# Optimization experiments

Hardware: AMD Instinct MI355X
Metric: run time of the kernel (lower is better)

## Reference

```python
import jax, jax.numpy as jnp
import numpy as np

E = 400000          # num edges
N_ATOMS = 16000     # num atoms
N_GRAPHS = 256      # num crystals in batch
D_EDGE = 128        # emb_size_edge (== emb_size)
D_RBF = 16          # emb_size_rbf
SILU_SCALE = 1.0 / 0.6  # gemnet ScaledSiLU


def setup_inputs() -> dict:
    key = jax.random.key(0)
    ks = jax.random.split(key, 10)
    edge_emb = jax.random.normal(ks[0], (E, D_EDGE), dtype=jnp.float32)
    distance_vec = jax.random.normal(ks[1], (E, 3), dtype=jnp.float32)
    lattice = jax.random.normal(ks[2], (N_GRAPHS, 3, 3), dtype=jnp.float32)
    rbf = jax.random.uniform(ks[3], (E, D_RBF), dtype=jnp.float32)
    edge_index = jax.random.randint(ks[4], (2, E), 0, N_ATOMS, dtype=jnp.int64)
    batch = jnp.sort(jax.random.randint(ks[5], (N_ATOMS,), 0, N_GRAPHS, dtype=jnp.int64))
    # learned params (gemnet Dense: bias=False)
    def w(k, fan_in, fan_out):
        return jax.random.normal(k, (fan_in, fan_out), dtype=jnp.float32) / np.sqrt(fan_in)
    W1 = w(ks[6], D_EDGE, D_EDGE)       # mlp dense 1 (ScaledSiLU)
    W2 = w(ks[7], D_EDGE, D_EDGE)       # mlp dense 2 (linear)
    W_rbf = w(ks[8], D_RBF, D_EDGE)     # dense_rbf_F
    W_out = w(ks[9], D_EDGE, 1)         # out_forces (num_heads=1)
    return {"edge_emb": edge_emb, "distance_vec": distance_vec, "lattice": lattice,
            "rbf": rbf, "W1": W1, "W2": W2, "W_rbf": W_rbf, "W_out": W_out,
            "edge_index": edge_index, "batch": batch}


def reference(edge_emb, distance_vec, lattice, rbf, W1, W2, W_rbf, W_out, edge_index, batch):
    num_graphs = lattice.shape[0]
    # compute_score_per_edge: MLP(edge_emb) gated by RBF embedding
    x_F = (jax.nn.silu(edge_emb @ W1) * SILU_SCALE) @ W2      # [E, D_EDGE]
    rbf_emb_F = rbf @ W_rbf                                    # [E, D_EDGE]
    edge_scores = (x_F * rbf_emb_F) @ W_out                    # [E, 1]
    # normalize_score=True: divide by number of edges in each graph
    batch_edge = batch[edge_index[0]]                          # [E] graph id per edge
    num_edges = jax.ops.segment_sum(jnp.ones((edge_scores.shape[0],), edge_scores.dtype),
                                    batch_edge, num_segments=num_graphs)
    edge_scores = edge_scores / num_edges[batch_edge][:, None]
    # edge_score_to_lattice_score_frac_symmetric (single head)
    s = edge_scores[:, 0]                                      # [E]
    unit = distance_vec / jnp.linalg.norm(distance_vec, axis=-1, keepdims=True)
    per_edge = jnp.einsum("e,ei,ej->eij", s, unit, distance_vec)  # [E,3,3]
    L = jax.ops.segment_sum(per_edge, batch_edge, num_segments=num_graphs)  # [B,3,3]
    L = 0.5 * (L + jnp.swapaxes(L, -1, -2))                    # symmetrize
    return L
```

## Files before the change

### kernel.cpp

```cpp
#include <hip/hip_runtime.h>
#include <hip/hip_bf16.h>

#define E_EDGES 400000
#define DE      128
#define DRBF    16
#define NG      256
#define TE      64
#define NTILES  (E_EDGES / TE)
#define SILU_SC (1.0f / 0.6f)
#define GRID_MAIN 1568

static_assert(E_EDGES % TE == 0, "tile divisibility");

typedef short bf16x8 __attribute__((ext_vector_type(8)));
typedef float f32x4  __attribute__((ext_vector_type(4)));

__device__ __forceinline__ unsigned int f2bf(float x) {
    union { float f; unsigned int u; } v; v.f = x;
    return (v.u + 0x7FFFu + ((v.u >> 16) & 1u)) >> 16;
}
__device__ __forceinline__ float silu_s(float h) {
    return h / (1.0f + __expf(-h)) * SILU_SC;
}


__global__ __launch_bounds__(256) void gn_prep(
    const float* __restrict__ W1, const float* __restrict__ W2,
    const float* __restrict__ Wr, const float* __restrict__ Wo,
    unsigned char* __restrict__ fragW1, unsigned char* __restrict__ fragG)
{
    const int tid = threadIdx.x, lane = tid & 63, wid = tid >> 6;
    const int lq = lane >> 4, lr = lane & 15, wcol = wid * 32;
    #pragma unroll
    for (int n = 0; n < 2; ++n) {
        const int col = wcol + n * 16 + lr;
        #pragma unroll
        for (int kt = 0; kt < 4; ++kt) {
            bf16x8 v;
            #pragma unroll
            for (int j = 0; j < 8; ++j)
                v[j] = (short)f2bf(W1[(kt * 32 + lq * 8 + j) * DE + col]);
            *reinterpret_cast<bf16x8*>(fragW1 + tid * 128 + (n * 4 + kt) * 16) = v;
        }
        bf16x8 vg = {0, 0, 0, 0, 0, 0, 0, 0};
        if (lq < 2) {
            #pragma unroll
            for (int jj = 0; jj < 8; ++jj) {
                const int j = lq * 8 + jj;
                f32x4 a4 = {0.0f, 0.0f, 0.0f, 0.0f};
                for (int c4 = 0; c4 < 32; ++c4) {
                    const f32x4 w2 = *reinterpret_cast<const f32x4*>(W2 + col * DE + c4 * 4);
                    const f32x4 wr = *reinterpret_cast<const f32x4*>(Wr + j * DE + c4 * 4);
                    const f32x4 wo = *reinterpret_cast<const f32x4*>(Wo + c4 * 4);
                    a4 += w2 * wr * wo;
                }
                vg[jj] = (short)f2bf(a4[0] + a4[1] + a4[2] + a4[3]);
            }
        }
        *reinterpret_cast<bf16x8*>(fragG + tid * 32 + n * 16) = vg;
    }
}

__global__ void gn_count(const int* __restrict__ ei0, const int* __restrict__ batch,
                         int* __restrict__ counts) {
    __shared__ int hist[NG];
    const int tid = threadIdx.x;
    hist[tid] = 0;
    __syncthreads();
    for (int e = blockIdx.x * 256 + tid; e < E_EDGES; e += gridDim.x * 256)
        atomicAdd(&hist[batch[ei0[e]]], 1);
    __syncthreads();
    if (hist[tid]) atomicAdd(&counts[tid], hist[tid]);
}

__global__ __launch_bounds__(256, 3) void gn_main(
    const float* __restrict__ edge_emb, const float* __restrict__ dvec,
    const float* __restrict__ rbf, const int* __restrict__ ei0,
    const int* __restrict__ batch, const int* __restrict__ counts,
    const unsigned char* __restrict__ fragW1, const unsigned char* __restrict__ fragG,
    float* __restrict__ Lws)
{
    __shared__ __align__(16) unsigned char sA[2][TE * DE * 2];
    __shared__ __align__(16) unsigned char sR[2][TE * DRBF * 2];
    __shared__ float sS[2][4][TE];
    __shared__ float sLacc[NG * 9];

    const int tid = threadIdx.x, lane = tid & 63, wid = tid >> 6;
    const int lq = lane >> 4, lr = lane & 15;

    for (int i = tid; i < NG * 9; i += 256) sLacc[i] = 0.0f;

    bf16x8 b1[2][4], bG[2];
    #pragma unroll
    for (int n = 0; n < 2; ++n) {
        #pragma unroll
        for (int kt = 0; kt < 4; ++kt)
            b1[n][kt] = *reinterpret_cast<const bf16x8*>(fragW1 + tid * 128 + (n * 4 + kt) * 16);
        bG[n] = *reinterpret_cast<const bf16x8*>(fragG + tid * 32 + n * 16);
    }

    const f32x4 zero4 = {0.0f, 0.0f, 0.0f, 0.0f};

    {
        const int t0 = blockIdx.x;
        if (t0 < NTILES) {
            const size_t e0 = (size_t)t0 * TE;
            #pragma unroll
            for (int i = 0; i < 8; ++i) {
                const int f4 = i * 256 + tid, row = f4 >> 5, c4 = (f4 & 31) << 2;
                const float4 v = *reinterpret_cast<const float4*>(edge_emb + (e0 + row) * DE + c4);
                uint2 p; p.x = f2bf(v.x) | (f2bf(v.y) << 16); p.y = f2bf(v.z) | (f2bf(v.w) << 16);
                *reinterpret_cast<uint2*>(&sA[0][(row * 256 + c4 * 2) ^ ((row & 7) << 4)]) = p;
            }
            const int row = tid >> 2, ch = tid & 3;
            const float4 v = *reinterpret_cast<const float4*>(rbf + (e0 + row) * DRBF + ch * 4);
            uint2 p; p.x = f2bf(v.x) | (f2bf(v.y) << 16); p.y = f2bf(v.z) | (f2bf(v.w) << 16);
            *reinterpret_cast<uint2*>(&sR[0][row * 32 + ch * 8]) = p;
        }
    }
    __syncthreads();

    int cur = 0;
    for (int t = blockIdx.x; t < NTILES; t += GRID_MAIN) {
        const int tn = t + GRID_MAIN;
        const bool pf = tn < NTILES;

        float4 ve[8], vr;
        if (pf) {
            const size_t e0n = (size_t)tn * TE;
            #pragma unroll
            for (int i = 0; i < 8; ++i) {
                const int f4 = i * 256 + tid, row = f4 >> 5, c4 = (f4 & 31) << 2;
                ve[i] = *reinterpret_cast<const float4*>(edge_emb + (e0n + row) * DE + c4);
            }
            vr = *reinterpret_cast<const float4*>(rbf + (e0n + (tid >> 2)) * DRBF + (tid & 3) * 4);
        }
        int g = 0; float cinv = 0.0f, dx = 0.0f, dy = 0.0f, dz = 0.0f;
        if (tid < TE) {
            const size_t e = (size_t)t * TE + tid;
            g = batch[ei0[e]];
            cinv = 1.0f / (float)counts[g];
            dx = dvec[3 * e]; dy = dvec[3 * e + 1]; dz = dvec[3 * e + 2];
        }

        f32x4 acc[4][2];
        #pragma unroll
        for (int m = 0; m < 4; ++m) { acc[m][0] = zero4; acc[m][1] = zero4; }
        #pragma unroll
        for (int kt = 0; kt < 4; ++kt) {
            bf16x8 a[4];
            #pragma unroll
            for (int m = 0; m < 4; ++m) {
                const int row = m * 16 + lr;
                a[m] = *reinterpret_cast<const bf16x8*>(
                    &sA[cur][(row * 256 + kt * 64 + lq * 16) ^ ((row & 7) << 4)]);
            }
            #pragma unroll
            for (int m = 0; m < 4; ++m) {
                acc[m][0] = __builtin_amdgcn_mfma_f32_16x16x32_bf16(a[m], b1[0][kt], acc[m][0], 0, 0, 0);
                acc[m][1] = __builtin_amdgcn_mfma_f32_16x16x32_bf16(a[m], b1[1][kt], acc[m][1], 0, 0, 0);
            }
        }

        #pragma unroll
        for (int m = 0; m < 4; ++m) {
            bf16x8 aR = {0, 0, 0, 0, 0, 0, 0, 0};
            if (lq < 2)
                aR = *reinterpret_cast<const bf16x8*>(&sR[cur][(m * 16 + lr) * 32 + lq * 16]);
            const f32x4 y0 = __builtin_amdgcn_mfma_f32_16x16x32_bf16(aR, bG[0], zero4, 0, 0, 0);
            const f32x4 y1 = __builtin_amdgcn_mfma_f32_16x16x32_bf16(aR, bG[1], zero4, 0, 0, 0);
            f32x4 p;
            #pragma unroll
            for (int r = 0; r < 4; ++r)
                p[r] = silu_s(acc[m][0][r]) * y0[r] + silu_s(acc[m][1][r]) * y1[r];
            #pragma unroll
            for (int off = 1; off < 16; off <<= 1)
                #pragma unroll
                for (int r = 0; r < 4; ++r)
                    p[r] += __shfl_xor(p[r], off, 64);
            if (lr == 0) {
                #pragma unroll
                for (int r = 0; r < 4; ++r)
                    sS[cur][wid][m * 16 + lq * 4 + r] = p[r];
            }
        }

        if (pf) {
            #pragma unroll
            for (int i = 0; i < 8; ++i) {
                const int f4 = i * 256 + tid, row = f4 >> 5, c4 = (f4 & 31) << 2;
                uint2 p; p.x = f2bf(ve[i].x) | (f2bf(ve[i].y) << 16);
                p.y = f2bf(ve[i].z) | (f2bf(ve[i].w) << 16);
                *reinterpret_cast<uint2*>(&sA[cur ^ 1][(row * 256 + c4 * 2) ^ ((row & 7) << 4)]) = p;
            }
            const int row = tid >> 2, ch = tid & 3;
            uint2 p; p.x = f2bf(vr.x) | (f2bf(vr.y) << 16); p.y = f2bf(vr.z) | (f2bf(vr.w) << 16);
            *reinterpret_cast<uint2*>(&sR[cur ^ 1][row * 32 + ch * 8]) = p;
        }

        __syncthreads();

        if (tid < TE) {
            float s = (sS[cur][0][tid] + sS[cur][1][tid] + sS[cur][2][tid] + sS[cur][3][tid]) * cinv;
            const float rn = 1.0f / sqrtf(dx * dx + dy * dy + dz * dz);
            const float sx = s * dx * rn, sy = s * dy * rn, sz = s * dz * rn;
            float* L = sLacc + g * 9;
            atomicAdd(L + 0, sx * dx); atomicAdd(L + 1, sx * dy); atomicAdd(L + 2, sx * dz);
            atomicAdd(L + 3, sy * dx); atomicAdd(L + 4, sy * dy); atomicAdd(L + 5, sy * dz);
            atomicAdd(L + 6, sz * dx); atomicAdd(L + 7, sz * dy); atomicAdd(L + 8, sz * dz);
        }
        cur ^= 1;
    }

    __syncthreads();
    for (int i = tid; i < NG * 9; i += 256)
        atomicAdd(&Lws[i], sLacc[i]);
}

__global__ void gn_finalize(const float* __restrict__ Lws, float* __restrict__ out) {
    const int i = blockIdx.x * 256 + threadIdx.x;
    if (i < NG * 9) {
        const int g = i / 9, rem = i % 9, r = rem / 3, c = rem % 3;
        out[i] = 0.5f * (Lws[i] + Lws[g * 9 + c * 3 + r]);
    }
}

extern "C" void kernel_launch(void* const* d_in, const int* in_sizes, int n_in,
                              void* d_out, int out_size, void* d_ws, size_t ws_size,
                              hipStream_t stream) {
    const float* edge_emb = (const float*)d_in[0];
    const float* dvec     = (const float*)d_in[1];
    const float* rbf      = (const float*)d_in[3];
    const float* W1       = (const float*)d_in[4];
    const float* W2       = (const float*)d_in[5];
    const float* Wr       = (const float*)d_in[6];
    const float* Wo       = (const float*)d_in[7];
    const int*   ei0      = (const int*)d_in[8];
    const int*   batch    = (const int*)d_in[9];
    float* out = (float*)d_out;

    int*   counts = (int*)d_ws;
    float* Lws    = (float*)((char*)d_ws + 1024);
    unsigned char* fragW1 = (unsigned char*)d_ws + 10240;
    unsigned char* fragG  = (unsigned char*)d_ws + 43008;

    hipMemsetAsync(d_ws, 0, 10240, stream);
    gn_prep<<<1, 256, 0, stream>>>(W1, W2, Wr, Wo, fragW1, fragG);
    gn_count<<<256, 256, 0, stream>>>(ei0, batch, counts);
    gn_main<<<GRID_MAIN, 256, 0, stream>>>(edge_emb, dvec, rbf, ei0, batch, counts,
                                           fragW1, fragG, Lws);
    gn_finalize<<<9, 256, 0, stream>>>(Lws, out);
}
```

Measured before the change: 491.4 us.

## Give each wavefront its own 16-edge tile with full W1 held in registers

The main kernel now assigns each wavefront an independent 16-edge tile and has it hold all of W1's bf16 fragments (8 column blocks by 4 k-steps) in registers. Edge embeddings are loaded from global memory straight into MFMA operand registers, which removes the LDS staging buffers, the double-buffer prefetch and the per-tile block barrier. The prep kernel is spread over 32 small blocks and the fused W2·Wrbf·Wout fragments are now read from global memory on each tile. In exchange, register pressure rises (occupancy hint drops from 3 to 2 blocks), there is no explicit prefetch, and edge rows are read with a less coalesced pattern that relies on the cache.

```diff
diff --git a/kernel.cpp b/kernel.cpp
--- a/kernel.cpp
+++ b/kernel.cpp
@@ -5,12 +5,12 @@
 #define DE      128
 #define DRBF    16
 #define NG      256
-#define TE      64
-#define NTILES  (E_EDGES / TE)
+#define MT      16
+#define NMT     (E_EDGES / MT)
 #define SILU_SC (1.0f / 0.6f)
-#define GRID_MAIN 1568
-
-static_assert(E_EDGES % TE == 0, "tile divisibility");
+#define GRID_MAIN 768
+
+static_assert(E_EDGES % MT == 0, "tile divisibility");
 
 typedef short bf16x8 __attribute__((ext_vector_type(8)));
 typedef float f32x4  __attribute__((ext_vector_type(4)));
@@ -19,45 +19,51 @@
     union { float f; unsigned int u; } v; v.f = x;
     return (v.u + 0x7FFFu + ((v.u >> 16) & 1u)) >> 16;
 }
+__device__ __forceinline__ bf16x8 cvt8(f32x4 a, f32x4 b) {
+    bf16x8 r;
+    #pragma unroll
+    for (int j = 0; j < 4; ++j) {
+        r[j]     = (short)f2bf(a[j]);
+        r[4 + j] = (short)f2bf(b[j]);
+    }
+    return r;
+}
 __device__ __forceinline__ float silu_s(float h) {
     return h / (1.0f + __expf(-h)) * SILU_SC;
 }
 
 
-__global__ __launch_bounds__(256) void gn_prep(
-    const float* __restrict__ W1, const float* __restrict__ W2,
-    const float* __restrict__ Wr, const float* __restrict__ Wo,
-    unsigned char* __restrict__ fragW1, unsigned char* __restrict__ fragG)
+__global__ void gn_prep(const float* __restrict__ W1, const float* __restrict__ W2,
+                        const float* __restrict__ Wr, const float* __restrict__ Wo,
+                        unsigned char* __restrict__ fragW1, unsigned char* __restrict__ fragG)
 {
-    const int tid = threadIdx.x, lane = tid & 63, wid = tid >> 6;
-    const int lq = lane >> 4, lr = lane & 15, wcol = wid * 32;
+    const int lane = threadIdx.x;
+    const int b = blockIdx.x;
+    const int n = b >> 2, kt = b & 3;
+    const int lq = lane >> 4, lr = lane & 15;
+
+    bf16x8 v;
     #pragma unroll
-    for (int n = 0; n < 2; ++n) {
-        const int col = wcol + n * 16 + lr;
-        #pragma unroll
-        for (int kt = 0; kt < 4; ++kt) {
-            bf16x8 v;
-            #pragma unroll
-            for (int j = 0; j < 8; ++j)
-                v[j] = (short)f2bf(W1[(kt * 32 + lq * 8 + j) * DE + col]);
-            *reinterpret_cast<bf16x8*>(fragW1 + tid * 128 + (n * 4 + kt) * 16) = v;
-        }
+    for (int j = 0; j < 8; ++j)
+        v[j] = (short)f2bf(W1[(kt * 32 + lq * 8 + j) * DE + n * 16 + lr]);
+    *reinterpret_cast<bf16x8*>(fragW1 + ((size_t)(b * 64 + lane)) * 16) = v;
+
+    if (kt == 0) {
         bf16x8 vg = {0, 0, 0, 0, 0, 0, 0, 0};
         if (lq < 2) {
+            const float* w2row = W2 + (n * 16 + lr) * DE;
             #pragma unroll
             for (int jj = 0; jj < 8; ++jj) {
-                const int j = lq * 8 + jj;
+                const float* wrrow = Wr + (lq * 8 + jj) * DE;
                 f32x4 a4 = {0.0f, 0.0f, 0.0f, 0.0f};
-                for (int c4 = 0; c4 < 32; ++c4) {
-                    const f32x4 w2 = *reinterpret_cast<const f32x4*>(W2 + col * DE + c4 * 4);
-                    const f32x4 wr = *reinterpret_cast<const f32x4*>(Wr + j * DE + c4 * 4);
-                    const f32x4 wo = *reinterpret_cast<const f32x4*>(Wo + c4 * 4);
-                    a4 += w2 * wr * wo;
-                }
+                for (int c4 = 0; c4 < 32; ++c4)
+                    a4 += *reinterpret_cast<const f32x4*>(w2row + c4 * 4)
+                        * *reinterpret_cast<const f32x4*>(wrrow + c4 * 4)
+                        * *reinterpret_cast<const f32x4*>(Wo + c4 * 4);
                 vg[jj] = (short)f2bf(a4[0] + a4[1] + a4[2] + a4[3]);
             }
         }
-        *reinterpret_cast<bf16x8*>(fragG + tid * 32 + n * 16) = vg;
+        *reinterpret_cast<bf16x8*>(fragG + ((size_t)(n * 64 + lane)) * 16) = vg;
     }
 }
 
@@ -73,135 +79,86 @@
     if (hist[tid]) atomicAdd(&counts[tid], hist[tid]);
 }
 
-__global__ __launch_bounds__(256, 3) void gn_main(
+__global__ __launch_bounds__(256, 2) void gn_main(
     const float* __restrict__ edge_emb, const float* __restrict__ dvec,
     const float* __restrict__ rbf, const int* __restrict__ ei0,
     const int* __restrict__ batch, const int* __restrict__ counts,
     const unsigned char* __restrict__ fragW1, const unsigned char* __restrict__ fragG,
     float* __restrict__ Lws)
 {
-    __shared__ __align__(16) unsigned char sA[2][TE * DE * 2];
-    __shared__ __align__(16) unsigned char sR[2][TE * DRBF * 2];
-    __shared__ float sS[2][4][TE];
     __shared__ float sLacc[NG * 9];
+    __shared__ float sSc[4][16];
 
     const int tid = threadIdx.x, lane = tid & 63, wid = tid >> 6;
     const int lq = lane >> 4, lr = lane & 15;
 
     for (int i = tid; i < NG * 9; i += 256) sLacc[i] = 0.0f;
 
-    bf16x8 b1[2][4], bG[2];
+    bf16x8 b1[8][4];
     #pragma unroll
-    for (int n = 0; n < 2; ++n) {
+    for (int n = 0; n < 8; ++n)
         #pragma unroll
         for (int kt = 0; kt < 4; ++kt)
-            b1[n][kt] = *reinterpret_cast<const bf16x8*>(fragW1 + tid * 128 + (n * 4 + kt) * 16);
-        bG[n] = *reinterpret_cast<const bf16x8*>(fragG + tid * 32 + n * 16);
-    }
+            b1[n][kt] = *reinterpret_cast<const bf16x8*>(fragW1 + ((size_t)((n * 4 + kt) * 64 + lane)) * 16);
+    __syncthreads();
 
     const f32x4 zero4 = {0.0f, 0.0f, 0.0f, 0.0f};
-
-    {
-        const int t0 = blockIdx.x;
-        if (t0 < NTILES) {
-            const size_t e0 = (size_t)t0 * TE;
-            #pragma unroll
-            for (int i = 0; i < 8; ++i) {
-                const int f4 = i * 256 + tid, row = f4 >> 5, c4 = (f4 & 31) << 2;
-                const float4 v = *reinterpret_cast<const float4*>(edge_emb + (e0 + row) * DE + c4);
-                uint2 p; p.x = f2bf(v.x) | (f2bf(v.y) << 16); p.y = f2bf(v.z) | (f2bf(v.w) << 16);
-                *reinterpret_cast<uint2*>(&sA[0][(row * 256 + c4 * 2) ^ ((row & 7) << 4)]) = p;
-            }
-            const int row = tid >> 2, ch = tid & 3;
-            const float4 v = *reinterpret_cast<const float4*>(rbf + (e0 + row) * DRBF + ch * 4);
-            uint2 p; p.x = f2bf(v.x) | (f2bf(v.y) << 16); p.y = f2bf(v.z) | (f2bf(v.w) << 16);
-            *reinterpret_cast<uint2*>(&sR[0][row * 32 + ch * 8]) = p;
-        }
-    }
-    __syncthreads();
-
-    int cur = 0;
-    for (int t = blockIdx.x; t < NTILES; t += GRID_MAIN) {
-        const int tn = t + GRID_MAIN;
-        const bool pf = tn < NTILES;
-
-        float4 ve[8], vr;
-        if (pf) {
-            const size_t e0n = (size_t)tn * TE;
-            #pragma unroll
-            for (int i = 0; i < 8; ++i) {
-                const int f4 = i * 256 + tid, row = f4 >> 5, c4 = (f4 & 31) << 2;
-                ve[i] = *reinterpret_cast<const float4*>(edge_emb + (e0n + row) * DE + c4);
-            }
-            vr = *reinterpret_cast<const float4*>(rbf + (e0n + (tid >> 2)) * DRBF + (tid & 3) * 4);
-        }
+    const int gw = blockIdx.x * 4 + wid;
+    const int nw = GRID_MAIN * 4;
+
+    for (int mt = gw; mt < NMT; mt += nw) {
+        const size_t e0 = (size_t)mt * MT;
+
         int g = 0; float cinv = 0.0f, dx = 0.0f, dy = 0.0f, dz = 0.0f;
-        if (tid < TE) {
-            const size_t e = (size_t)t * TE + tid;
+        if (lane < 16) {
+            const size_t e = e0 + lane;
             g = batch[ei0[e]];
             cinv = 1.0f / (float)counts[g];
             dx = dvec[3 * e]; dy = dvec[3 * e + 1]; dz = dvec[3 * e + 2];
         }
 
-        f32x4 acc[4][2];
-        #pragma unroll
-        for (int m = 0; m < 4; ++m) { acc[m][0] = zero4; acc[m][1] = zero4; }
+        bf16x8 aR = {0, 0, 0, 0, 0, 0, 0, 0};
+        if (lq < 2) {
+            const float* rp = rbf + (e0 + lr) * DRBF + lq * 8;
+            aR = cvt8(*reinterpret_cast<const f32x4*>(rp),
+                      *reinterpret_cast<const f32x4*>(rp + 4));
+        }
+
+        f32x4 acc[8];
+        #pragma unroll
+        for (int n = 0; n < 8; ++n) acc[n] = zero4;
+        const float* ap = edge_emb + (e0 + lr) * DE + lq * 8;
         #pragma unroll
         for (int kt = 0; kt < 4; ++kt) {
-            bf16x8 a[4];
-            #pragma unroll
-            for (int m = 0; m < 4; ++m) {
-                const int row = m * 16 + lr;
-                a[m] = *reinterpret_cast<const bf16x8*>(
-                    &sA[cur][(row * 256 + kt * 64 + lq * 16) ^ ((row & 7) << 4)]);
-            }
-            #pragma unroll
-            for (int m = 0; m < 4; ++m) {
-                acc[m][0] = __builtin_amdgcn_mfma_f32_16x16x32_bf16(a[m], b1[0][kt], acc[m][0], 0, 0, 0);
-                acc[m][1] = __builtin_amdgcn_mfma_f32_16x16x32_bf16(a[m], b1[1][kt], acc[m][1], 0, 0, 0);
-            }
-        }
-
-        #pragma unroll
-        for (int m = 0; m < 4; ++m) {
-            bf16x8 aR = {0, 0, 0, 0, 0, 0, 0, 0};
-            if (lq < 2)
-                aR = *reinterpret_cast<const bf16x8*>(&sR[cur][(m * 16 + lr) * 32 + lq * 16]);
-            const f32x4 y0 = __builtin_amdgcn_mfma_f32_16x16x32_bf16(aR, bG[0], zero4, 0, 0, 0);
-            const f32x4 y1 = __builtin_amdgcn_mfma_f32_16x16x32_bf16(aR, bG[1], zero4, 0, 0, 0);
-            f32x4 p;
+            const bf16x8 a = cvt8(*reinterpret_cast<const f32x4*>(ap + kt * 32),
+                                  *reinterpret_cast<const f32x4*>(ap + kt * 32 + 4));
+            #pragma unroll
+            for (int n = 0; n < 8; ++n)
+                acc[n] = __builtin_amdgcn_mfma_f32_16x16x32_bf16(a, b1[n][kt], acc[n], 0, 0, 0);
+        }
+
+        f32x4 p = zero4;
+        #pragma unroll
+        for (int n = 0; n < 8; ++n) {
+            const bf16x8 bg = *reinterpret_cast<const bf16x8*>(fragG + ((size_t)(n * 64 + lane)) * 16);
+            const f32x4 y = __builtin_amdgcn_mfma_f32_16x16x32_bf16(aR, bg, zero4, 0, 0, 0);
             #pragma unroll
             for (int r = 0; r < 4; ++r)
-                p[r] = silu_s(acc[m][0][r]) * y0[r] + silu_s(acc[m][1][r]) * y1[r];
-            #pragma unroll
-            for (int off = 1; off < 16; off <<= 1)
-                #pragma unroll
-                for (int r = 0; r < 4; ++r)
-                    p[r] += __shfl_xor(p[r], off, 64);
-            if (lr == 0) {
-                #pragma unroll
-                for (int r = 0; r < 4; ++r)
-                    sS[cur][wid][m * 16 + lq * 4 + r] = p[r];
-            }
-        }
-
-        if (pf) {
-            #pragma unroll
-            for (int i = 0; i < 8; ++i) {
-                const int f4 = i * 256 + tid, row = f4 >> 5, c4 = (f4 & 31) << 2;
-                uint2 p; p.x = f2bf(ve[i].x) | (f2bf(ve[i].y) << 16);
-                p.y = f2bf(ve[i].z) | (f2bf(ve[i].w) << 16);
-                *reinterpret_cast<uint2*>(&sA[cur ^ 1][(row * 256 + c4 * 2) ^ ((row & 7) << 4)]) = p;
-            }
-            const int row = tid >> 2, ch = tid & 3;
-            uint2 p; p.x = f2bf(vr.x) | (f2bf(vr.y) << 16); p.y = f2bf(vr.z) | (f2bf(vr.w) << 16);
-            *reinterpret_cast<uint2*>(&sR[cur ^ 1][row * 32 + ch * 8]) = p;
-        }
-
-        __syncthreads();
-
-        if (tid < TE) {
-            float s = (sS[cur][0][tid] + sS[cur][1][tid] + sS[cur][2][tid] + sS[cur][3][tid]) * cinv;
+                p[r] += silu_s(acc[n][r]) * y[r];
+        }
+        #pragma unroll
+        for (int off = 1; off < 16; off <<= 1)
+            #pragma unroll
+            for (int r = 0; r < 4; ++r)
+                p[r] += __shfl_xor(p[r], off, 64);
+
+        if (lr == 0) {
+            #pragma unroll
+            for (int r = 0; r < 4; ++r)
+                sSc[wid][lq * 4 + r] = p[r];
+        }
+        if (lane < 16) {
+            const float s = sSc[wid][lane] * cinv;
             const float rn = 1.0f / sqrtf(dx * dx + dy * dy + dz * dz);
             const float sx = s * dx * rn, sy = s * dy * rn, sz = s * dz * rn;
             float* L = sLacc + g * 9;
@@ -209,7 +166,6 @@
             atomicAdd(L + 3, sy * dx); atomicAdd(L + 4, sy * dy); atomicAdd(L + 5, sy * dz);
             atomicAdd(L + 6, sz * dx); atomicAdd(L + 7, sz * dy); atomicAdd(L + 8, sz * dz);
         }
-        cur ^= 1;
     }
 
     __syncthreads();
@@ -245,7 +201,7 @@
     unsigned char* fragG  = (unsigned char*)d_ws + 43008;
 
     hipMemsetAsync(d_ws, 0, 10240, stream);
-    gn_prep<<<1, 256, 0, stream>>>(W1, W2, Wr, Wo, fragW1, fragG);
+    gn_prep<<<32, 64, 0, stream>>>(W1, W2, Wr, Wo, fragW1, fragG);
     gn_count<<<256, 256, 0, stream>>>(ei0, batch, counts);
     gn_main<<<GRID_MAIN, 256, 0, stream>>>(edge_emb, dvec, rbf, ei0, batch, counts,
                                            fragW1, fragG, Lws);
```

After: 405.1 us. 17.6% less time.
